# Optimization experiments

Measured on AMD Instinct MI355X. Metric: run time of the kernel, lower is better.

The kernel has to match this reference:

```python
import jax, jax.numpy as jnp
import numpy as np

A_LO = 0      # interval lower bound
B_HI = 63     # interval upper bound -> window W = 64
PAD_BIG = 1.0e4  # finite pad so exp(-scale*PAD_BIG) == 0 exactly in fp32 (no inf/nan grads)


def setup_inputs() -> dict:
    key = jax.random.key(0)
    k1, k2 = jax.random.split(key)
    B, T = 64, 2048
    phi = jax.random.normal(k1, (B, T, 2), dtype=jnp.float32)
    psi = jax.random.normal(k2, (B, T, 2), dtype=jnp.float32)
    return {"phi": phi, "psi": psi, "scale": 8}


def reference(phi, psi, scale):
    # phi, psi: [B, T, 2] robustness traces of left/right subformulas.
    a, b = A_LO, B_HI
    Bsz, T, _ = phi.shape
    W = b - a + 1
    s = jnp.float32(scale)

    # Pad time axis so every window of length W fits. phi padded with a large
    # value (neutral for smooth-min), psi with a large negative value (neutral
    # for smooth-max); both exactly neutral in fp32 since exp(-s*1e4) == 0.
    phi_pad = jnp.pad(phi, ((0, 0), (0, b), (0, 0)), constant_values=PAD_BIG)
    psi_pad = jnp.pad(psi, ((0, 0), (0, b), (0, 0)), constant_values=-PAD_BIG)

    # tau = t + a + j, j in [0, W)
    idx = jnp.arange(T)[:, None] + jnp.arange(a, b + 1)[None, :]  # [T, W]
    phi_win = phi_pad[:, idx]  # [B, T, W, 2], phi at t+k
    psi_win = psi_pad[:, idx]  # [B, T, W, 2], psi at tau

    # Smooth min over phi[t : tau] (exclusive of tau):
    #   min_phi(k) = -logsumexp_{s'=t..t+k-1}(-s*phi[s']) / s
    # computed via a cumulative logsumexp over the window axis.
    neg = -s * phi_win
    cumlse = jax.lax.associative_scan(jnp.logaddexp, neg, axis=2)  # [B,T,W,2]
    shifted = jnp.concatenate(
        [jnp.zeros_like(cumlse[:, :, :1]), cumlse[:, :, :-1]], axis=2)
    k_off = jnp.arange(W)[None, None, :, None] + a  # tau - t
    # tau == t -> min over empty segment -> ones (per original code)
    min_phi = jnp.where(k_off == 0, jnp.float32(1.0), -shifted / s)

    # Smooth min of the pair {min_phi, psi[tau]}
    cand = -jnp.logaddexp(-s * min_phi, -s * psi_win) / s  # [B,T,W,2]

    # Mask tau > T-1 (candidates that don't exist in the original loop).
    valid = (jnp.arange(T)[:, None] + a + jnp.arange(W)[None, :]) <= (T - 1)
    cand = jnp.where(valid[None, :, :, None], cand, -PAD_BIG)

    # Smooth max over candidate taus
    best = jax.nn.logsumexp(s * cand, axis=2) / s  # [B, T, 2]
    return best
```

## Files before the change

### kernel.cpp

```cpp
#include <hip/hip_runtime.h>
#include <math.h>


#define T_DIM   2048
#define W_WIN   64
#define BLOCK_T 256
#define STAGE   (BLOCK_T + W_WIN - 1)

__global__ __launch_bounds__(BLOCK_T) void until_kernel(
    const float* __restrict__ phi,
    const float* __restrict__ psi,
    const int*  __restrict__ scale_p,
    float* __restrict__ out)
{
    __shared__ float4 s_d[STAGE];

    const int b   = blockIdx.y;
    const int t0  = blockIdx.x * BLOCK_T;
    const int tid = threadIdx.x;
    const float s  = (float)(*scale_p);
    const float ns = -s;

    const float2* __restrict__ phi2 = (const float2*)(phi + (size_t)b * T_DIM * 2);
    const float2* __restrict__ psi2 = (const float2*)(psi + (size_t)b * T_DIM * 2);

    for (int i = tid; i < STAGE; i += BLOCK_T) {
        int t = t0 + i;
        float4 v;
        if (t < T_DIM) {
            float2 pv = phi2[t];
            float2 qv = psi2[t];
            v.x = __expf(ns * pv.x);
            v.y = __expf(ns * pv.y);
            v.z = __expf(ns * qv.x);
            v.w = __expf(ns * qv.y);
        } else {
            v.x = 0.f; v.y = 0.f;
            v.z = INFINITY; v.w = INFINITY;
        }
        s_d[i] = v;
    }
    __syncthreads();

    const float Es = __expf(ns);

    float4 v0 = s_d[tid];
    float accA0 = __builtin_amdgcn_rcpf(Es + v0.z);
    float accA1 = __builtin_amdgcn_rcpf(Es + v0.w);
    float accB0 = 0.f, accB1 = 0.f;
    float sum0 = v0.x;
    float sum1 = v0.y;

    #pragma unroll
    for (int k = 1; k < W_WIN; ++k) {
        float4 v = s_d[tid + k];
        float r0 = __builtin_amdgcn_rcpf(sum0 + v.z);
        float r1 = __builtin_amdgcn_rcpf(sum1 + v.w);
        if (k & 1) { accA0 += r0; accA1 += r1; }
        else       { accB0 += r0; accB1 += r1; }
        sum0 += v.x;
        sum1 += v.y;
    }

    const int t = t0 + tid;
    float2* __restrict__ out2 = (float2*)(out + (size_t)b * T_DIM * 2);
    out2[t] = make_float2(__logf(accA0 + accB0) / s, __logf(accA1 + accB1) / s);
}

extern "C" void kernel_launch(void* const* d_in, const int* in_sizes, int n_in,
                              void* d_out, int out_size, void* d_ws, size_t ws_size,
                              hipStream_t stream) {
    const float* phi   = (const float*)d_in[0];
    const float* psi   = (const float*)d_in[1];
    const int*   scale = (const int*)d_in[2];
    float* out = (float*)d_out;

    const int B = in_sizes[0] / (T_DIM * 2);
    dim3 grid(T_DIM / BLOCK_T, B);
    until_kernel<<<grid, dim3(BLOCK_T), 0, stream>>>(phi, psi, scale, out);
}
```

Measured before the change: 61.46 us.

## Compute two adjacent timesteps per thread sharing window loads

```diff
diff --git a/kernel.cpp b/kernel.cpp
--- a/kernel.cpp
+++ b/kernel.cpp
@@ -2,21 +2,24 @@
 #include <math.h>
 
 
-#define T_DIM   2048
-#define W_WIN   64
-#define BLOCK_T 256
-#define STAGE   (BLOCK_T + W_WIN - 1)
+#define T_DIM    2048
+#define W_WIN    64
+#define TILE     512
+#define NTHREADS 256
+#define STAGE    (TILE + W_WIN)
+#define HALF     (STAGE / 2)
 
-__global__ __launch_bounds__(BLOCK_T) void until_kernel(
+__global__ __launch_bounds__(NTHREADS) void until_kernel(
     const float* __restrict__ phi,
     const float* __restrict__ psi,
     const int*  __restrict__ scale_p,
     float* __restrict__ out)
 {
-    __shared__ float4 s_d[STAGE];
+    __shared__ float4 s_e[HALF];
+    __shared__ float4 s_o[HALF];
 
     const int b   = blockIdx.y;
-    const int t0  = blockIdx.x * BLOCK_T;
+    const int t0  = blockIdx.x * TILE;
     const int tid = threadIdx.x;
     const float s  = (float)(*scale_p);
     const float ns = -s;
@@ -24,7 +27,7 @@
     const float2* __restrict__ phi2 = (const float2*)(phi + (size_t)b * T_DIM * 2);
     const float2* __restrict__ psi2 = (const float2*)(psi + (size_t)b * T_DIM * 2);
 
-    for (int i = tid; i < STAGE; i += BLOCK_T) {
+    for (int i = tid; i < STAGE; i += NTHREADS) {
         int t = t0 + i;
         float4 v;
         if (t < T_DIM) {
@@ -38,33 +41,58 @@
             v.x = 0.f; v.y = 0.f;
             v.z = INFINITY; v.w = INFINITY;
         }
-        s_d[i] = v;
+        if (i & 1) s_o[i >> 1] = v;
+        else       s_e[i >> 1] = v;
     }
     __syncthreads();
 
     const float Es = __expf(ns);
 
-    float4 v0 = s_d[tid];
-    float accA0 = __builtin_amdgcn_rcpf(Es + v0.z);
-    float accA1 = __builtin_amdgcn_rcpf(Es + v0.w);
-    float accB0 = 0.f, accB1 = 0.f;
-    float sum0 = v0.x;
-    float sum1 = v0.y;
+
+    float4 va = s_e[tid];
+    float accA0 = __builtin_amdgcn_rcpf(Es + va.z);
+    float accA1 = __builtin_amdgcn_rcpf(Es + va.w);
+    float sumA0 = va.x, sumA1 = va.y;
+
+    float4 vb = s_o[tid];
+    float accB0 = __builtin_amdgcn_rcpf(Es + vb.z);
+    float accB1 = __builtin_amdgcn_rcpf(Es + vb.w);
+    accA0 += __builtin_amdgcn_rcpf(sumA0 + vb.z);
+    accA1 += __builtin_amdgcn_rcpf(sumA1 + vb.w);
+    sumA0 += vb.x; sumA1 += vb.y;
+    float sumB0 = vb.x, sumB1 = vb.y;
 
     #pragma unroll
-    for (int k = 1; k < W_WIN; ++k) {
-        float4 v = s_d[tid + k];
-        float r0 = __builtin_amdgcn_rcpf(sum0 + v.z);
-        float r1 = __builtin_amdgcn_rcpf(sum1 + v.w);
-        if (k & 1) { accA0 += r0; accA1 += r1; }
-        else       { accB0 += r0; accB1 += r1; }
-        sum0 += v.x;
-        sum1 += v.y;
+    for (int h = 1; h <= 31; ++h) {
+        float4 v = s_e[tid + h];
+        accA0 += __builtin_amdgcn_rcpf(sumA0 + v.z);
+        accA1 += __builtin_amdgcn_rcpf(sumA1 + v.w);
+        accB0 += __builtin_amdgcn_rcpf(sumB0 + v.z);
+        accB1 += __builtin_amdgcn_rcpf(sumB1 + v.w);
+        sumA0 += v.x; sumA1 += v.y;
+        sumB0 += v.x; sumB1 += v.y;
+
+        float4 u = s_o[tid + h];
+        accA0 += __builtin_amdgcn_rcpf(sumA0 + u.z);
+        accA1 += __builtin_amdgcn_rcpf(sumA1 + u.w);
+        accB0 += __builtin_amdgcn_rcpf(sumB0 + u.z);
+        accB1 += __builtin_amdgcn_rcpf(sumB1 + u.w);
+        sumA0 += u.x; sumA1 += u.y;
+        sumB0 += u.x; sumB1 += u.y;
     }
 
-    const int t = t0 + tid;
-    float2* __restrict__ out2 = (float2*)(out + (size_t)b * T_DIM * 2);
-    out2[t] = make_float2(__logf(accA0 + accB0) / s, __logf(accA1 + accB1) / s);
+    float4 vz = s_e[tid + 32];
+    accB0 += __builtin_amdgcn_rcpf(sumB0 + vz.z);
+    accB1 += __builtin_amdgcn_rcpf(sumB1 + vz.w);
+
+    const float inv_s = 1.0f / s;
+    float4 o;
+    o.x = __logf(accA0) * inv_s;
+    o.y = __logf(accA1) * inv_s;
+    o.z = __logf(accB0) * inv_s;
+    o.w = __logf(accB1) * inv_s;
+    float4* __restrict__ out4 = (float4*)(out + (size_t)b * T_DIM * 2);
+    out4[(t0 >> 1) + tid] = o;
 }
 
 extern "C" void kernel_launch(void* const* d_in, const int* in_sizes, int n_in,
@@ -76,6 +104,6 @@
     float* out = (float*)d_out;
 
     const int B = in_sizes[0] / (T_DIM * 2);
-    dim3 grid(T_DIM / BLOCK_T, B);
-    until_kernel<<<grid, dim3(BLOCK_T), 0, stream>>>(phi, psi, scale, out);
+    dim3 grid(T_DIM / TILE, B);
+    until_kernel<<<grid, dim3(NTHREADS), 0, stream>>>(phi, psi, scale, out);
 }
```

New measurement: 61.46 us. No clear change (+0.0%).
